# Optimization experiments

Hardware: AMD Instinct MI355X
Metric: run time of the kernel (lower is better)

The kernel has to match this reference:

```python
import jax, jax.numpy as jnp
import numpy as np

B, N, DIM = 2, 2048, 1024
HEADS, DIM_HEAD = 16, 64
INNER = HEADS * DIM_HEAD  # 1024


def setup_inputs() -> dict:
    key = jax.random.key(0)
    k1, k2, k3, k4 = jax.random.split(key, 4)
    x = jax.random.normal(k1, (B, N, DIM), dtype=jnp.float32)
    # Linear weights (stored as [in, out] so y = x @ W)
    Wq = jax.random.normal(k2, (DIM, INNER), dtype=jnp.float32) * (DIM ** -0.5)
    Wkv = jax.random.normal(k3, (DIM, INNER * 2), dtype=jnp.float32) * (DIM ** -0.5)
    Wo = jax.random.normal(k4, (INNER, DIM), dtype=jnp.float32) * (INNER ** -0.5)
    return {"x": x, "Wq": Wq, "Wkv": Wkv, "Wo": Wo}


def reference(x, Wq, Wkv, Wo):
    # q/k/v projections (no bias), split heads: b n (h d) -> b h n d
    b, n, _ = x.shape
    q = (x @ Wq).reshape(b, n, HEADS, DIM_HEAD).transpose(0, 2, 1, 3)
    kv = x @ Wkv
    k, v = jnp.split(kv, 2, axis=-1)
    k = k.reshape(b, n, HEADS, DIM_HEAD).transpose(0, 2, 1, 3)
    v = v.reshape(b, n, HEADS, DIM_HEAD).transpose(0, 2, 1, 3)

    scale = DIM_HEAD ** -0.5
    scores = jnp.einsum('bhid,bhjd->bhij', q, k) * scale  # [b,h,n,n]
    # causal mask: positions j > i masked with most-negative value (as in torch impl)
    max_neg = -jnp.finfo(scores.dtype).max
    causal_mask = jnp.triu(jnp.ones((n, n), dtype=bool), k=1)
    scores = jnp.where(causal_mask, max_neg, scores)
    p = jax.nn.softmax(scores, axis=-1)
    out = jnp.einsum('bhij,bhjd->bhid', p, v)  # [b,h,n,d]
    out = out.transpose(0, 2, 1, 3).reshape(b, n, INNER)
    return out @ Wo
```

## Files before the change

kernel.cpp:

```cpp
#include <hip/hip_runtime.h>
#include <cstdint>


typedef __bf16 bf16_t;
typedef __bf16 bf16x8 __attribute__((ext_vector_type(8)));
typedef __bf16 bf16x4 __attribute__((ext_vector_type(4)));
typedef float  f32x4  __attribute__((ext_vector_type(4)));
typedef float  f32x16 __attribute__((ext_vector_type(16)));
typedef unsigned int u32;

#define QSCALE 0.18033688011112042f


__device__ __forceinline__ float fast_exp2(float x) {
#if __has_builtin(__builtin_amdgcn_exp2f)
  return __builtin_amdgcn_exp2f(x);
#else
  return exp2f(x);
#endif
}

__device__ __forceinline__ void swap32(u32& a, u32& b) {
#if __has_builtin(__builtin_amdgcn_permlane32_swap)
  typedef unsigned int u32x2 __attribute__((ext_vector_type(2)));
  const u32x2 r = __builtin_amdgcn_permlane32_swap(a, b, false, false);
  a = r[0]; b = r[1];
#else
  const u32 xa = (u32)__shfl_xor((int)a, 32, 64);
  const u32 xb = (u32)__shfl_xor((int)b, 32, 64);
  const bool hi = (threadIdx.x & 32) != 0;
  const u32 r0 = hi ? xb : a;
  const u32 r1 = hi ? b : xa;
  a = r0; b = r1;
#endif
}

__device__ __forceinline__ void gload_lds16(const void* gsrc, void* ldst) {
  __builtin_amdgcn_global_load_lds(
      (__attribute__((address_space(1))) void*)(uintptr_t)gsrc,
      (__attribute__((address_space(3))) void*)(uintptr_t)(uint32_t)(uintptr_t)ldst,
      16, 0, 0);
}

__device__ __forceinline__ u32 pkbf(float a, float b) {
  const u32 lo = (u32)__builtin_bit_cast(unsigned short, (bf16_t)a);
  const u32 hi = (u32)__builtin_bit_cast(unsigned short, (bf16_t)b);
  return (hi << 16) | lo;
}

__global__ __launch_bounds__(256) void cvt_kernel(const float* __restrict__ in,
                                                  bf16_t* __restrict__ out) {
  const int idx = (blockIdx.x * 256 + threadIdx.x) * 4;
  const float4 v = *(const float4*)(in + idx);
  bf16x4 o;
  o[0] = (bf16_t)v.x; o[1] = (bf16_t)v.y; o[2] = (bf16_t)v.z; o[3] = (bf16_t)v.w;
  *(bf16x4*)(out + idx) = o;
}

__global__ __launch_bounds__(256) void transpose_kernel(const float* __restrict__ W,
                                                        bf16_t* __restrict__ Wt,
                                                        int K, int Nn) {
  __shared__ float tile[32][33];
  const int bx = blockIdx.x, by = blockIdx.y;
  const int x = bx * 32 + threadIdx.x;
  #pragma unroll
  for (int r0 = 0; r0 < 32; r0 += 8) {
    const int r = r0 + threadIdx.y;
    tile[r][threadIdx.x] = W[(size_t)(by * 32 + r) * Nn + x];
  }
  __syncthreads();
  const int xo = by * 32 + threadIdx.x;
  #pragma unroll
  for (int r0 = 0; r0 < 32; r0 += 8) {
    const int r = r0 + threadIdx.y;
    Wt[(size_t)(bx * 32 + r) * K + xo] = (bf16_t)tile[threadIdx.x][r];
  }
}

template <int MODE, int BN>
__global__ __launch_bounds__(256) void gemm_kernel(
    const bf16_t* __restrict__ A, const bf16_t* __restrict__ Bt,
    bf16_t* __restrict__ outQ, bf16_t* __restrict__ outK,
    bf16_t* __restrict__ outV, float* __restrict__ outf) {
  constexpr int KD = 1024;
  constexpr int NB = BN / 32;
  constexpr int NW = BN / 2;
  constexpr int NACC = NW / 16;
  __shared__ bf16_t As[2][128][64];
  __shared__ bf16_t Bs[2][BN][64];
  const int t = threadIdx.x;
  const int lane = t & 63, w = t >> 6;
  const int wr = w >> 1, wc = w & 1;
  const int lrow = lane & 15, lq = lane >> 4;
  const int bm = blockIdx.y * 128, bn = blockIdx.x * BN;

  f32x4 acc[4][NACC] = {};

  auto stage = [&](int buf, int k0) {
    #pragma unroll
    for (int i = 0; i < 4; ++i) {
      const int lin = i * 256 + t;
      const int row = lin >> 3;
      const int sc = (lin & 7) ^ (row & 7);
      gload_lds16(A + (size_t)(bm + row) * KD + k0 + sc * 8,
                  &As[buf][0][0] + lin * 8);
    }
    #pragma unroll
    for (int i = 0; i < NB; ++i) {
      const int lin = i * 256 + t;
      const int row = lin >> 3;
      const int sc = (lin & 7) ^ (row & 7);
      gload_lds16(Bt + (size_t)(bn + row) * KD + k0 + sc * 8,
                  &Bs[buf][0][0] + lin * 8);
    }
  };

  stage(0, 0);
  for (int kt = 0; kt < KD / 64; ++kt) {
    const int cur = kt & 1;
    if (kt + 1 < KD / 64) {
      stage(cur ^ 1, (kt + 1) * 64);
      if constexpr (BN == 128)
        asm volatile("s_waitcnt vmcnt(8)" ::: "memory");
      else
        asm volatile("s_waitcnt vmcnt(6)" ::: "memory");
    } else {
      asm volatile("s_waitcnt vmcnt(0)" ::: "memory");
    }
    __builtin_amdgcn_s_barrier();

    #pragma unroll
    for (int kk = 0; kk < 2; ++kk) {
      bf16x8 aF[4], bF[NACC];
      #pragma unroll
      for (int m = 0; m < 4; ++m) {
        const int row = wr * 64 + m * 16 + lrow;
        const int ch = (kk * 4 + lq) ^ (row & 7);
        aF[m] = *(const bf16x8*)&As[cur][row][ch * 8];
      }
      #pragma unroll
      for (int n = 0; n < NACC; ++n) {
        const int row = wc * NW + n * 16 + lrow;
        const int ch = (kk * 4 + lq) ^ (row & 7);
        bF[n] = *(const bf16x8*)&Bs[cur][row][ch * 8];
      }
      #pragma unroll
      for (int m = 0; m < 4; ++m)
        #pragma unroll
        for (int n = 0; n < NACC; ++n)
          acc[m][n] = __builtin_amdgcn_mfma_f32_16x16x32_bf16(aF[m], bF[n],
                                                              acc[m][n], 0, 0, 0);
    }
    asm volatile("s_waitcnt lgkmcnt(0)" ::: "memory");
    __builtin_amdgcn_s_barrier();
  }

  if constexpr (MODE == 2) {
    #pragma unroll
    for (int m = 0; m < 4; ++m) {
      const int ri = bm + wr * 64 + m * 16 + lq * 4;
      #pragma unroll
      for (int n = 0; n < NACC; ++n) {
        const int ci = bn + wc * NW + n * 16 + lrow;
        const f32x4 v = acc[m][n];
        #pragma unroll
        for (int r = 0; r < 4; ++r)
          outf[(size_t)(ri + r) * 1024 + ci] = v[r];
      }
    }
  } else if (bn < 2048) {
    bf16_t* Cs = (bf16_t*)&As[0][0][0];
    bf16_t* dst = (bn < 1024) ? outQ : outK;
    const float sc = (bn < 1024) ? QSCALE : 1.0f;
    #pragma unroll
    for (int m = 0; m < 4; ++m) {
      const int rr0 = wr * 64 + m * 16 + lq * 4;
      #pragma unroll
      for (int n = 0; n < NACC; ++n) {
        const int c = wc * NW + n * 16 + lrow;
        const int hh = c >> 6, d = c & 63;
        const f32x4 v = acc[m][n];
        #pragma unroll
        for (int r = 0; r < 4; ++r) {
          const int rr = rr0 + r;
          const int off = ((hh * 2 + (rr >> 6)) << 12)
                        + (((d >> 4) * 2 + ((rr >> 5) & 1)) << 9)
                        + ((((d >> 3) & 1) * 32 + (rr & 31)) << 3) + (d & 7);
          Cs[off] = (bf16_t)(v[r] * sc);
        }
      }
    }
    __syncthreads();
    const int b = bm >> 11;
    const int qc0 = (bm & 2047) >> 6;
    const int h0 = (bn & 1023) >> 6;
    #pragma unroll
    for (int chk = 0; chk < 4; ++chk) {
      const int hh = chk >> 1, qc = chk & 1;
      bf16_t* gb = dst + (size_t)(b * 16 + h0 + hh) * 131072
                 + (size_t)(qc0 + qc) * 4096;
      #pragma unroll
      for (int it = 0; it < 2; ++it) {
        const int e = (it * 256 + t) * 8;
        *(bf16x8*)(gb + e) = *(const bf16x8*)(Cs + chk * 4096 + e);
      }
    }
  } else {
    #pragma unroll
    for (int m = 0; m < 4; ++m) {
      const int ri = bm + wr * 64 + m * 16 + lq * 4;
      #pragma unroll
      for (int n = 0; n < NACC; ++n) {
        const int ci = bn + wc * NW + n * 16 + lrow;
        const f32x4 v = acc[m][n];
        const int hd = ci - 2048;
        const int h = hd >> 6, d = hd & 63;
        const int b = ri >> 11, j0 = ri & 2047;
        bf16x4 pk;
        pk[0] = (bf16_t)v[0]; pk[1] = (bf16_t)v[1];
        pk[2] = (bf16_t)v[2]; pk[3] = (bf16_t)v[3];
        const size_t elem = (size_t)(b * 16 + h) * 131072
            + (size_t)((j0 >> 6) * 8 + ((j0 & 63) >> 4) * 2 + (d >> 5)) * 512
            + ((((j0 >> 3) & 1) * 32) + (d & 31)) * 8 + (j0 & 7);
        *(bf16x4*)(outV + elem) = pk;
      }
    }
  }
}

__global__ void __attribute__((amdgpu_flat_work_group_size(256, 256),
                               amdgpu_waves_per_eu(4, 4)))
attn_kernel(
    const bf16_t* __restrict__ Qf, const bf16_t* __restrict__ Kf,
    const bf16_t* __restrict__ Vf, bf16_t* __restrict__ Ow) {
  const int t = threadIdx.x;
  const int lane = t & 63, w = t >> 6;
  const int l31 = lane & 31, hi = lane >> 5;
  const int G = ((blockIdx.x & 7) << 7) + (blockIdx.x >> 3);
  const int bh = G >> 5;
  const int p = G & 31;
  const int qsA = 63 - p, qsB = p;
  const int ntA = (qsA >> 1) + 1, ntB = (qsB >> 1) + 1;
  const int wA = min(3, (4 * ntA + ((ntA + ntB) >> 1)) / (ntA + ntB));
  const bool isA = (w < wA);
  const int qs = isA ? qsA : qsB;
  const int nt = isA ? ntA : ntB;
  const int widx = isA ? w : (w - wA);
  const int ws = isA ? wA : (4 - wA);
  const int qg = qs * 32 + l31;
  const bf16_t* Qb = Qf + (size_t)bh * 131072 + (size_t)(qs >> 1) * 4096 + (qs & 1) * 512;
  const bf16_t* Kb = Kf + (size_t)bh * 131072;
  const bf16_t* Vb = Vf + (size_t)bh * 131072;

  bf16x8 qf[4];
  #pragma unroll
  for (int ks = 0; ks < 4; ++ks)
    qf[ks] = *(const bf16x8*)(Qb + ks * 1024 + lane * 8);

  f32x16 acc0 = {}, acc1 = {};
  float m_run = -1e30f, l_half = 0.f;

  for (int jt = widx; jt < nt; jt += ws) {
    const bf16_t* Kt = Kb + (size_t)jt * 4096;
    const bf16_t* Vt = Vb + (size_t)jt * 4096;

    bf16x8 kc[8];
    #pragma unroll
    for (int f = 0; f < 8; ++f)
      kc[f] = *(const bf16x8*)(Kt + f * 512 + lane * 8);

    f32x16 st0 = {}, st1 = {};
    #pragma unroll
    for (int ks = 0; ks < 4; ++ks) {
      st0 = __builtin_amdgcn_mfma_f32_32x32x16_bf16(kc[2 * ks], qf[ks], st0, 0, 0, 0);
      st1 = __builtin_amdgcn_mfma_f32_32x32x16_bf16(kc[2 * ks + 1], qf[ks], st1, 0, 0, 0);
    }

    if (jt == nt - 1) {
      const int thr = qg - jt * 64;
      #pragma unroll
      for (int r = 0; r < 16; ++r) {
        const int jl = (r & 3) + 8 * (r >> 2) + 4 * hi;
        st0[r] = (jl > thr) ? -1e30f : st0[r];
        st1[r] = (32 + jl > thr) ? -1e30f : st1[r];
      }
    }

    float t8[8];
    #pragma unroll
    for (int i = 0; i < 8; ++i)
      t8[i] = fmaxf(fmaxf(st0[i], st0[i + 8]), fmaxf(st1[i], st1[i + 8]));
    #pragma unroll
    for (int i = 0; i < 4; ++i) t8[i] = fmaxf(t8[i], t8[i + 4]);
    const float pmax = fmaxf(fmaxf(t8[0], t8[1]), fmaxf(t8[2], t8[3]));

    if (!__all(pmax <= m_run + 8.0f)) {
      const float mx = fmaxf(pmax, __shfl_xor(pmax, 32, 64));
      const float m_new = fmaxf(m_run, mx);
      const float corr = fast_exp2(m_run - m_new);
      m_run = m_new;
      l_half *= corr;
      #pragma unroll
      for (int r = 0; r < 16; ++r) { acc0[r] *= corr; acc1[r] *= corr; }
    }

    #pragma unroll
    for (int r = 0; r < 16; ++r) {
      st0[r] = fast_exp2(st0[r] - m_run);
      st1[r] = fast_exp2(st1[r] - m_run);
    }
    float s8[8];
    #pragma unroll
    for (int i = 0; i < 8; ++i)
      s8[i] = (st0[i] + st0[i + 8]) + (st1[i] + st1[i + 8]);
    #pragma unroll
    for (int i = 0; i < 4; ++i) s8[i] += s8[i + 4];
    l_half += (s8[0] + s8[1]) + (s8[2] + s8[3]);

    bf16x8 vf[8];
    #pragma unroll
    for (int f = 0; f < 8; ++f)
      vf[f] = *(const bf16x8*)(Vt + f * 512 + lane * 8);

    u32 Wa[8], Wb[8];
    #pragma unroll
    for (int g = 0; g < 8; ++g) {
      Wa[g] = pkbf(st0[2 * g], st0[2 * g + 1]);
      Wb[g] = pkbf(st1[2 * g], st1[2 * g + 1]);
    }
    swap32(Wa[0], Wa[2]); swap32(Wa[1], Wa[3]);
    swap32(Wa[4], Wa[6]); swap32(Wa[5], Wa[7]);
    swap32(Wb[0], Wb[2]); swap32(Wb[1], Wb[3]);
    swap32(Wb[4], Wb[6]); swap32(Wb[5], Wb[7]);
    const uint4 u0 = make_uint4(Wa[0], Wa[1], Wa[2], Wa[3]);
    const uint4 u1 = make_uint4(Wa[4], Wa[5], Wa[6], Wa[7]);
    const uint4 u2 = make_uint4(Wb[0], Wb[1], Wb[2], Wb[3]);
    const uint4 u3 = make_uint4(Wb[4], Wb[5], Wb[6], Wb[7]);
    const bf16x8 pf0 = __builtin_bit_cast(bf16x8, u0);
    const bf16x8 pf1 = __builtin_bit_cast(bf16x8, u1);
    const bf16x8 pf2 = __builtin_bit_cast(bf16x8, u2);
    const bf16x8 pf3 = __builtin_bit_cast(bf16x8, u3);

    #pragma unroll
    for (int tt = 0; tt < 4; ++tt) {
      const bf16x8 pf = tt == 0 ? pf0 : tt == 1 ? pf1 : tt == 2 ? pf2 : pf3;
      acc0 = __builtin_amdgcn_mfma_f32_32x32x16_bf16(vf[2 * tt], pf, acc0, 0, 0, 0);
      acc1 = __builtin_amdgcn_mfma_f32_32x32x16_bf16(vf[2 * tt + 1], pf, acc1, 0, 0, 0);
    }
  }

  const float l_wave = l_half + __shfl_xor(l_half, 32, 64);

  __shared__ float mO[2][32][64];
  __shared__ float mML[2][2][64];
  const bool leader = (w == 0) || (w == wA);
  if (!leader) {
    const int slot = isA ? (w - 1) : (wA - 1 + (w - wA - 1));
    mML[0][slot][lane] = m_run;
    mML[1][slot][lane] = l_wave;
    #pragma unroll
    for (int r = 0; r < 16; ++r) {
      mO[slot][r][lane] = acc0[r];
      mO[slot][16 + r][lane] = acc1[r];
    }
  }
  __syncthreads();
  if (leader) {
    const int base = isA ? 0 : (wA - 1);
    const int nsl = ws - 1;
    float mk[2], lk[2], ck[2];
    float mt = m_run;
    for (int k = 0; k < nsl; ++k) {
      mk[k] = mML[0][base + k][lane];
      lk[k] = mML[1][base + k][lane];
      mt = fmaxf(mt, mk[k]);
    }
    const float c0 = fast_exp2(m_run - mt);
    float l = l_wave * c0;
    for (int k = 0; k < nsl; ++k) {
      ck[k] = fast_exp2(mk[k] - mt);
      l += lk[k] * ck[k];
    }
    const float inv = 1.0f / l;
    const int b = bh >> 4, h = bh & 15;
    bf16_t* Obase = Ow + (((size_t)(b * 2048 + qg)) << 10) + h * 64;
    #pragma unroll
    for (int g = 0; g < 4; ++g) {
      bf16x4 p0, p1;
      #pragma unroll
      for (int j = 0; j < 4; ++j) {
        float a0 = acc0[4 * g + j] * c0;
        float a1 = acc1[4 * g + j] * c0;
        for (int k = 0; k < nsl; ++k) {
          a0 += mO[base + k][4 * g + j][lane] * ck[k];
          a1 += mO[base + k][16 + 4 * g + j][lane] * ck[k];
        }
        p0[j] = (bf16_t)(a0 * inv);
        p1[j] = (bf16_t)(a1 * inv);
      }
      *(bf16x4*)(Obase + 8 * g + 4 * hi) = p0;
      *(bf16x4*)(Obase + 32 + 8 * g + 4 * hi) = p1;
    }
  }
}

extern "C" void kernel_launch(void* const* d_in, const int* in_sizes, int n_in,
                              void* d_out, int out_size, void* d_ws, size_t ws_size,
                              hipStream_t stream) {
  const float* x   = (const float*)d_in[0];
  const float* Wq  = (const float*)d_in[1];
  const float* Wkv = (const float*)d_in[2];
  const float* Wo  = (const float*)d_in[3];
  float* out = (float*)d_out;
  char* ws = (char*)d_ws;

  const size_t MB = 1024 * 1024;
  bf16_t* Xbf   = (bf16_t*)(ws);
  bf16_t* Wqkvt = (bf16_t*)(ws + 8 * MB);
  bf16_t* Wot   = (bf16_t*)(ws + 14 * MB);
  bf16_t* Qw    = (bf16_t*)(ws + 16 * MB);
  bf16_t* Kw    = (bf16_t*)(ws + 24 * MB);
  bf16_t* Vtw   = (bf16_t*)(ws + 32 * MB);
  bf16_t* Aw    = (bf16_t*)(ws + 40 * MB);

  cvt_kernel<<<4096, 256, 0, stream>>>(x, Xbf);
  dim3 tb(32, 8);
  transpose_kernel<<<dim3(32, 32), tb, 0, stream>>>(Wq, Wqkvt, 1024, 1024);
  transpose_kernel<<<dim3(64, 32), tb, 0, stream>>>(Wkv, Wqkvt + 1024 * 1024, 1024, 2048);
  transpose_kernel<<<dim3(32, 32), tb, 0, stream>>>(Wo, Wot, 1024, 1024);

  gemm_kernel<1, 128><<<dim3(24, 32), 256, 0, stream>>>(Xbf, Wqkvt, Qw, Kw, Vtw, nullptr);
  attn_kernel<<<1024, 256, 0, stream>>>(Qw, Kw, Vtw, Aw);
  gemm_kernel<2, 64><<<dim3(16, 32), 256, 0, stream>>>(Aw, Wot, nullptr, nullptr, nullptr, out);
}
```

Before: 101.8 us.

## Fuse input conversion and weight transposes into one prep kernel; prefetch next K tile

Merges the x fp32-to-bf16 conversion and the three weight transpose launches into a single prep kernel that dispatches on block index, removing three kernel launches and their gaps. Separately, the attention loop now loads the next K tile into registers right after issuing the current QK MFMAs, so global load latency overlaps the softmax and PV work. The prefetch keeps the K fragments live across the whole iteration, which raises register pressure and could lower occupancy. The __syncthreads sits inside a block-uniform branch, so it stays correct.

```diff
diff --git a/kernel.cpp b/kernel.cpp
--- a/kernel.cpp
+++ b/kernel.cpp
@@ -48,32 +48,41 @@
   return (hi << 16) | lo;
 }
 
-__global__ __launch_bounds__(256) void cvt_kernel(const float* __restrict__ in,
-                                                  bf16_t* __restrict__ out) {
-  const int idx = (blockIdx.x * 256 + threadIdx.x) * 4;
-  const float4 v = *(const float4*)(in + idx);
-  bf16x4 o;
-  o[0] = (bf16_t)v.x; o[1] = (bf16_t)v.y; o[2] = (bf16_t)v.z; o[3] = (bf16_t)v.w;
-  *(bf16x4*)(out + idx) = o;
-}
-
-__global__ __launch_bounds__(256) void transpose_kernel(const float* __restrict__ W,
-                                                        bf16_t* __restrict__ Wt,
-                                                        int K, int Nn) {
-  __shared__ float tile[32][33];
-  const int bx = blockIdx.x, by = blockIdx.y;
-  const int x = bx * 32 + threadIdx.x;
-  #pragma unroll
-  for (int r0 = 0; r0 < 32; r0 += 8) {
-    const int r = r0 + threadIdx.y;
-    tile[r][threadIdx.x] = W[(size_t)(by * 32 + r) * Nn + x];
-  }
-  __syncthreads();
-  const int xo = by * 32 + threadIdx.x;
-  #pragma unroll
-  for (int r0 = 0; r0 < 32; r0 += 8) {
-    const int r = r0 + threadIdx.y;
-    Wt[(size_t)(bx * 32 + r) * K + xo] = (bf16_t)tile[threadIdx.x][r];
+__global__ __launch_bounds__(256) void prep_kernel(
+    const float* __restrict__ x, const float* __restrict__ Wq,
+    const float* __restrict__ Wkv, const float* __restrict__ Wo,
+    bf16_t* __restrict__ Xbf, bf16_t* __restrict__ Wqkvt,
+    bf16_t* __restrict__ Wot) {
+  const int bid = blockIdx.x;
+  if (bid < 4096) {
+    const int idx = (bid * 256 + threadIdx.x) * 4;
+    const float4 v = *(const float4*)(x + idx);
+    bf16x4 o;
+    o[0] = (bf16_t)v.x; o[1] = (bf16_t)v.y; o[2] = (bf16_t)v.z; o[3] = (bf16_t)v.w;
+    *(bf16x4*)(Xbf + idx) = o;
+  } else {
+    const int tb = bid - 4096;
+    const float* W; bf16_t* Wt; int Nn, bx, by;
+    if (tb < 1024)      { W = Wq;  Wt = Wqkvt;                Nn = 1024; bx = tb & 31; by = tb >> 5; }
+    else if (tb < 3072) { const int u = tb - 1024;
+                          W = Wkv; Wt = Wqkvt + 1024 * 1024;  Nn = 2048; bx = u & 63;  by = u >> 6; }
+    else                { const int u = tb - 3072;
+                          W = Wo;  Wt = Wot;                  Nn = 1024; bx = u & 31;  by = u >> 5; }
+    __shared__ float tile[32][33];
+    const int tx = threadIdx.x & 31, ty = threadIdx.x >> 5;
+    const int xcol = bx * 32 + tx;
+    #pragma unroll
+    for (int r0 = 0; r0 < 32; r0 += 8) {
+      const int r = r0 + ty;
+      tile[r][tx] = W[(size_t)(by * 32 + r) * Nn + xcol];
+    }
+    __syncthreads();
+    const int xo = by * 32 + tx;
+    #pragma unroll
+    for (int r0 = 0; r0 < 32; r0 += 8) {
+      const int r = r0 + ty;
+      Wt[(size_t)(bx * 32 + r) * 1024 + xo] = (bf16_t)tile[tx][r];
+    }
   }
 }
 
@@ -260,20 +269,30 @@
   f32x16 acc0 = {}, acc1 = {};
   float m_run = -1e30f, l_half = 0.f;
 
+  bf16x8 kc[8];
+  if (widx < nt) {
+    const bf16_t* K0 = Kb + (size_t)widx * 4096;
+    #pragma unroll
+    for (int f = 0; f < 8; ++f)
+      kc[f] = *(const bf16x8*)(K0 + f * 512 + lane * 8);
+  }
+
   for (int jt = widx; jt < nt; jt += ws) {
-    const bf16_t* Kt = Kb + (size_t)jt * 4096;
     const bf16_t* Vt = Vb + (size_t)jt * 4096;
-
-    bf16x8 kc[8];
-    #pragma unroll
-    for (int f = 0; f < 8; ++f)
-      kc[f] = *(const bf16x8*)(Kt + f * 512 + lane * 8);
 
     f32x16 st0 = {}, st1 = {};
     #pragma unroll
     for (int ks = 0; ks < 4; ++ks) {
       st0 = __builtin_amdgcn_mfma_f32_32x32x16_bf16(kc[2 * ks], qf[ks], st0, 0, 0, 0);
       st1 = __builtin_amdgcn_mfma_f32_32x32x16_bf16(kc[2 * ks + 1], qf[ks], st1, 0, 0, 0);
+    }
+
+    const int jn = jt + ws;
+    if (jn < nt) {
+      const bf16_t* Kn = Kb + (size_t)jn * 4096;
+      #pragma unroll
+      for (int f = 0; f < 8; ++f)
+        kc[f] = *(const bf16x8*)(Kn + f * 512 + lane * 8);
     }
 
     if (jt == nt - 1) {
@@ -423,12 +442,7 @@
   bf16_t* Vtw   = (bf16_t*)(ws + 32 * MB);
   bf16_t* Aw    = (bf16_t*)(ws + 40 * MB);
 
-  cvt_kernel<<<4096, 256, 0, stream>>>(x, Xbf);
-  dim3 tb(32, 8);
-  transpose_kernel<<<dim3(32, 32), tb, 0, stream>>>(Wq, Wqkvt, 1024, 1024);
-  transpose_kernel<<<dim3(64, 32), tb, 0, stream>>>(Wkv, Wqkvt + 1024 * 1024, 1024, 2048);
-  transpose_kernel<<<dim3(32, 32), tb, 0, stream>>>(Wo, Wot, 1024, 1024);
-
+  prep_kernel<<<8192, 256, 0, stream>>>(x, Wq, Wkv, Wo, Xbf, Wqkvt, Wot);
   gemm_kernel<1, 128><<<dim3(24, 32), 256, 0, stream>>>(Xbf, Wqkvt, Qw, Kw, Vtw, nullptr);
   attn_kernel<<<1024, 256, 0, stream>>>(Qw, Kw, Vtw, Aw);
   gemm_kernel<2, 64><<<dim3(16, 32), 256, 0, stream>>>(Aw, Wot, nullptr, nullptr, nullptr, out);
```

Result: slower. 159.2 us (+56.4%).
